# Kernel optimization log

Hardware: AMD Instinct MI355X
Metric: run time of the kernel (lower is better)

## Reference

```python
import jax, jax.numpy as jnp
import numpy as np

NF1, NF2, HEADS = 64, 64, 8
SCALE = (0.5 * (NF1 + NF2)) ** (-0.5)
EPS = 1e-5


def _ln(x, g, b):
    # LayerNorm over last axis
    mu = jnp.mean(x, axis=-1, keepdims=True)
    var = jnp.mean(jnp.square(x - mu), axis=-1, keepdims=True)
    return (x - mu) * jax.lax.rsqrt(var + EPS) * g + b


def setup_inputs() -> dict:
    key = jax.random.key(0)
    ks = jax.random.split(key, 16)
    B, H, W = 4, 256, 256
    s = 0.05
    return {
        "x1": jax.random.normal(ks[0], (B, NF1, H, W), jnp.float32),
        "x2": jax.random.normal(ks[1], (B, NF2, H, W), jnp.float32),
        "q_w": jax.random.normal(ks[2], (HEADS, NF1), jnp.float32) * s,
        "q_b": jnp.zeros((HEADS,), jnp.float32),
        "k_w": jax.random.normal(ks[3], (HEADS, NF2), jnp.float32) * s,
        "k_b": jnp.zeros((HEADS,), jnp.float32),
        "v_w": jax.random.normal(ks[4], (HEADS, NF1), jnp.float32) * s,
        "v_b": jnp.zeros((HEADS,), jnp.float32),
        "bias": jax.random.normal(ks[5], (1, 1, 1, NF2), jnp.float32),
        "sel_w": jax.random.normal(ks[6], (HEADS, NF2), jnp.float32) * s,
        "sel_b": jnp.zeros((HEADS,), jnp.float32),
        "fan_w": jax.random.normal(ks[7], (NF1, HEADS), jnp.float32) * s,
        "fan_b": jnp.zeros((NF1,), jnp.float32),
        "gamma": jax.random.normal(ks[8], (1, NF1, 1, 1), jnp.float32),
        "ln1_w": jnp.ones((NF1,), jnp.float32),
        "ln1_b": jnp.zeros((NF1,), jnp.float32),
        "ln2_w": jnp.ones((NF2,), jnp.float32),
        "ln2_b": jnp.zeros((NF2,), jnp.float32),
    }


def reference(x1, x2, q_w, q_b, k_w, k_b, v_w, v_b, bias, sel_w, sel_b,
              fan_w, fan_b, gamma, ln1_w, ln1_b, ln2_w, ln2_b):
    # Work in NHWC internally (matches the permute(0,2,3,1) pattern).
    x1n = _ln(jnp.transpose(x1, (0, 2, 3, 1)), ln1_w, ln1_b)  # [B,H,W,nf1]
    x2n = _ln(jnp.transpose(x2, (0, 2, 3, 1)), ln2_w, ln2_b)  # [B,H,W,nf2]

    # 1x1 convs == per-pixel linear projections
    q = jnp.einsum('bhwc,dc->bhwd', x1n, q_w) + q_b  # [B,H,W,heads]
    k = jnp.einsum('bhwc,dc->bhwd', x2n, k_w) + k_b  # [B,H,W,heads]
    v = jnp.einsum('bhwc,dc->bhwd', x1n, v_w) + v_b  # [B,H,W,heads]

    # row-wise attention over W: scores [B,H,W,W]
    attn = jax.nn.softmax(SCALE * jnp.einsum('bhwd,bhud->bhwu', q, k), axis=-1)
    mp = jnp.einsum('bhwu,bhud->bhwd', attn, v)  # [B,H,W,heads]

    # bias selector: Linear(nf2 -> heads) applied to learned bias [1,1,1,nf2]
    mp = mp + (jnp.einsum('ijkc,dc->ijkd', bias, sel_w) + sel_b)

    fo = jnp.einsum('bhwd,od->bhwo', mp, fan_w) + fan_b  # [B,H,W,nf1]
    g = jnp.transpose(gamma, (0, 2, 3, 1))  # [1,1,1,nf1]
    out = x1n + g * fo
    return jnp.transpose(out, (0, 3, 1, 2))  # NCHW [B,nf1,H,W]
```

## Files before the change

kernel.cpp:

```cpp
#include <hip/hip_runtime.h>

#define BDIM 512
#define HH 256
#define WW 256
#define NF 64
#define NH 8
#define HW (HH * WW)
#define WBP 68

typedef __attribute__((ext_vector_type(8))) short short8v;
typedef __attribute__((ext_vector_type(4))) float f32x4;

__device__ __forceinline__ unsigned short f2bf(float f) {
  const unsigned u = __float_as_uint(f);
  return (unsigned short)((u + 0x7fffu + ((u >> 16) & 1u)) >> 16);
}

__device__ __forceinline__ uint2 exp2_pack(f32x4 sv) {
  const float e0 = __builtin_amdgcn_exp2f(sv.x);
  const float e1 = __builtin_amdgcn_exp2f(sv.y);
  const float e2 = __builtin_amdgcn_exp2f(sv.z);
  const float e3 = __builtin_amdgcn_exp2f(sv.w);
  uint2 r;
  r.x = (unsigned)f2bf(e0) | ((unsigned)f2bf(e1) << 16);
  r.y = (unsigned)f2bf(e2) | ((unsigned)f2bf(e3) << 16);
  return r;
}

struct __align__(16) Smem {
  unsigned short kb16[WW * 8];
  unsigned short qb16[WW * 8];
  unsigned short vb16[8][264];
  union {
    struct { unsigned short wb1[16 * WBP]; unsigned short wb2[16 * WBP]; } w;
    float mpst[WW][10];
  } u1;
  union {
    unsigned short pstage[8][640];
    float murst2[WW][2];
  } u2;
  float murst[WW][2];
  float Sq1[NH], Sq0[NH], Sk1[NH], Sk0[NH], Sv1[NH], Sv0[NH], bsel[NH];
};

__global__ __launch_bounds__(BDIM, 6)
void cc_attn_kernel(const float* __restrict__ x1,
                    const float* __restrict__ x2,
                    const float* __restrict__ q_w,
                    const float* __restrict__ q_b,
                    const float* __restrict__ k_w,
                    const float* __restrict__ k_b,
                    const float* __restrict__ v_w,
                    const float* __restrict__ v_b,
                    const float* __restrict__ bias,
                    const float* __restrict__ sel_w,
                    const float* __restrict__ sel_b,
                    const float* __restrict__ fan_w,
                    const float* __restrict__ fan_b,
                    const float* __restrict__ gma,
                    const float* __restrict__ ln1w,
                    const float* __restrict__ ln1b,
                    const float* __restrict__ ln2w,
                    const float* __restrict__ ln2b,
                    float* __restrict__ out)
{
  __shared__ Smem s;
  const int tid  = threadIdx.x;
  const int lane = tid & 63;
  const int wid  = tid >> 6;
  const int g    = lane >> 4;
  const int r16  = lane & 15;
  const int b = blockIdx.x >> 8;
  const int h = blockIdx.x & 255;
  const size_t rowbase = ((size_t)(b * NF) * HH + h) * WW;

  const float QS = 0.125f * 1.44269504088896340736f;
  const short8v zero8 = {0,0,0,0,0,0,0,0};
  const f32x4 zero4 = {0.f, 0.f, 0.f, 0.f};

  if (tid < NH) {
    const int d = tid;
    float s1q = 0, s0q = 0, s1k = 0, s0k = 0, s1v = 0, s0v = 0, bs = 0;
    for (int c = 0; c < NF; c++) {
      const float qw = q_w[d * NF + c], kw = k_w[d * NF + c], vw = v_w[d * NF + c];
      s1q += ln1w[c] * qw; s0q += ln1b[c] * qw;
      s1k += ln2w[c] * kw; s0k += ln2b[c] * kw;
      s1v += ln1w[c] * vw; s0v += ln1b[c] * vw;
      bs  += bias[c] * sel_w[d * NF + c];
    }
    s.Sq1[d] = s1q; s.Sq0[d] = s0q + q_b[d];
    s.Sk1[d] = s1k; s.Sk0[d] = s0k + k_b[d];
    s.Sv1[d] = s1v; s.Sv0[d] = s0v + v_b[d];
    s.bsel[d] = bs + sel_b[d];
  }

  for (int i = tid; i < 16 * NF; i += BDIM) {
    const int n = i >> 6, c = i & 63;
    const float w1 = (n < 8 ? q_w[n * NF + c] : v_w[(n - 8) * NF + c]) * ln1w[c];
    const float w2 = (n < 8 ? k_w[n * NF + c] * ln2w[c] : 0.f);
    s.u1.w.wb1[n * WBP + c] = f2bf(w1);
    s.u1.w.wb2[n * WBP + c] = f2bf(w2);
  }

  __syncthreads();

  f32x4 accQV0 = zero4, accQV1 = zero4;
  float s1[2] = {0.f, 0.f}, q1[2] = {0.f, 0.f};

  #pragma unroll 1
  for (int kc = 0; kc < 2; ++kc) {
    const short8v bqv = *reinterpret_cast<const short8v*>(&s.u1.w.wb1[r16 * WBP + kc * 32 + g * 8]);
    #pragma unroll
    for (int m = 0; m < 2; ++m) {
      const int gp = wid * 32 + m * 16 + r16;
      const float* p1 = x1 + rowbase + gp + (size_t)(kc * 32 + g * 8) * HW;
      float xv[8];
      #pragma unroll
      for (int i = 0; i < 8; ++i) xv[i] = p1[(size_t)i * HW];
      unsigned short pk1[8];
      float la = 0.f, lb = 0.f;
      #pragma unroll
      for (int i = 0; i < 8; ++i) { la += xv[i]; lb += xv[i] * xv[i]; pk1[i] = f2bf(xv[i]); }
      s1[m] += la; q1[m] += lb;
      const short8v a1 = *reinterpret_cast<const short8v*>(pk1);
      if (m == 0) accQV0 = __builtin_amdgcn_mfma_f32_16x16x32_bf16(a1, bqv, accQV0, 0, 0, 0);
      else        accQV1 = __builtin_amdgcn_mfma_f32_16x16x32_bf16(a1, bqv, accQV1, 0, 0, 0);
    }
  }

  f32x4 accK0 = zero4, accK1 = zero4;
  float s2[2] = {0.f, 0.f}, q2p[2] = {0.f, 0.f};
  #pragma unroll 1
  for (int kc = 0; kc < 2; ++kc) {
    const short8v bk = *reinterpret_cast<const short8v*>(&s.u1.w.wb2[r16 * WBP + kc * 32 + g * 8]);
    #pragma unroll
    for (int m = 0; m < 2; ++m) {
      const int gp = wid * 32 + m * 16 + r16;
      const float* p2 = x2 + rowbase + gp + (size_t)(kc * 32 + g * 8) * HW;
      float yv[8];
      #pragma unroll
      for (int i = 0; i < 8; ++i) yv[i] = p2[(size_t)i * HW];
      unsigned short pk2[8];
      float lc = 0.f, ld = 0.f;
      #pragma unroll
      for (int i = 0; i < 8; ++i) { lc += yv[i]; ld += yv[i] * yv[i]; pk2[i] = f2bf(yv[i]); }
      s2[m] += lc; q2p[m] += ld;
      const short8v a2 = *reinterpret_cast<const short8v*>(pk2);
      if (m == 0) accK0 = __builtin_amdgcn_mfma_f32_16x16x32_bf16(a2, bk, accK0, 0, 0, 0);
      else        accK1 = __builtin_amdgcn_mfma_f32_16x16x32_bf16(a2, bk, accK1, 0, 0, 0);
    }
  }

  #pragma unroll
  for (int m = 0; m < 2; ++m) {
    float a = s1[m] + __shfl_xor(s1[m], 16);   a += __shfl_xor(a, 32);
    float v = q1[m] + __shfl_xor(q1[m], 16);   v += __shfl_xor(v, 32);
    float c = s2[m] + __shfl_xor(s2[m], 16);   c += __shfl_xor(c, 32);
    float d = q2p[m] + __shfl_xor(q2p[m], 16); d += __shfl_xor(d, 32);
    if (g == 0) {
      const int gp = wid * 32 + m * 16 + r16;
      const float mu1v = a * (1.f / NF);
      s.murst[gp][0] = mu1v;
      s.murst[gp][1] = rsqrtf(v * (1.f / NF) - mu1v * mu1v + 1e-5f);
      const float mu2v = c * (1.f / NF);
      s.u2.murst2[gp][0] = mu2v;
      s.u2.murst2[gp][1] = rsqrtf(d * (1.f / NF) - mu2v * mu2v + 1e-5f);
    }
  }

  __syncthreads();

  #pragma unroll
  for (int m = 0; m < 2; ++m) {
    const f32x4 aQV = m ? accQV1 : accQV0;
    const f32x4 aK  = m ? accK1  : accK0;
    #pragma unroll
    for (int j = 0; j < 4; ++j) {
      const int pix = wid * 32 + m * 16 + g * 4 + j;
      const float mu1v = s.murst[pix][0], rs1v = s.murst[pix][1];
      if (r16 < 8) {
        const float mu2v = s.u2.murst2[pix][0], rs2v = s.u2.murst2[pix][1];
        const float qv = (rs1v * (aQV[j] - mu1v * s.Sq1[r16]) + s.Sq0[r16]) * QS;
        s.qb16[pix * 8 + r16] = f2bf(qv);
        const float kv = rs2v * (aK[j] - mu2v * s.Sk1[r16]) + s.Sk0[r16];
        s.kb16[pix * 8 + r16] = f2bf(kv);
      } else {
        const float vv = rs1v * (aQV[j] - mu1v * s.Sv1[r16 - 8]) + s.Sv0[r16 - 8];
        s.vb16[r16 - 8][pix] = f2bf(vv);
      }
    }
  }

  __syncthreads();

  {
    const int qb0 = wid * 32;
    const short8v ones8 = {(short)0x3F80,(short)0x3F80,(short)0x3F80,(short)0x3F80,
                           (short)0x3F80,(short)0x3F80,(short)0x3F80,(short)0x3F80};

    short8v bq0 = zero8, bq1 = zero8;
    if (g == 0) {
      bq0 = *reinterpret_cast<const short8v*>(&s.qb16[(qb0 + r16) * 8]);
      bq1 = *reinterpret_cast<const short8v*>(&s.qb16[(qb0 + 16 + r16) * 8]);
    }

    f32x4 o0 = zero4, o1 = zero4;
    unsigned short* __restrict__ pst = &s.u2.pstage[wid][0];
    const int wr_off = r16 * 40 + g * 4;
    const int rd_off = r16 * 40 + g * 8;

    #pragma unroll 2
    for (int ch = 0; ch < 8; ++ch) {
      const int u0 = ch * 32;
      short8v ak0 = zero8, ak1 = zero8;
      if (g == 0) {
        ak0 = *reinterpret_cast<const short8v*>(&s.kb16[(u0 + r16) * 8]);
        ak1 = *reinterpret_cast<const short8v*>(&s.kb16[(u0 + 16 + r16) * 8]);
      }
      short8v av = zero8;
      if (r16 < 8)       av = *reinterpret_cast<const short8v*>(&s.vb16[r16][u0 + g * 8]);
      else if (r16 == 8) av = ones8;

      {
        f32x4 s0 = __builtin_amdgcn_mfma_f32_16x16x32_bf16(ak0, bq0, zero4, 0, 0, 0);
        f32x4 s1v = __builtin_amdgcn_mfma_f32_16x16x32_bf16(ak1, bq0, zero4, 0, 0, 0);
        const uint2 p0 = exp2_pack(s0);
        const uint2 p1 = exp2_pack(s1v);
        *reinterpret_cast<uint2*>(&pst[wr_off])      = p0;
        *reinterpret_cast<uint2*>(&pst[wr_off + 16]) = p1;
        const short8v bp = *reinterpret_cast<const short8v*>(&pst[rd_off]);
        o0 = __builtin_amdgcn_mfma_f32_16x16x32_bf16(av, bp, o0, 0, 0, 0);
      }
      {
        f32x4 s0 = __builtin_amdgcn_mfma_f32_16x16x32_bf16(ak0, bq1, zero4, 0, 0, 0);
        f32x4 s1v = __builtin_amdgcn_mfma_f32_16x16x32_bf16(ak1, bq1, zero4, 0, 0, 0);
        const uint2 p0 = exp2_pack(s0);
        const uint2 p1 = exp2_pack(s1v);
        *reinterpret_cast<uint2*>(&pst[wr_off])      = p0;
        *reinterpret_cast<uint2*>(&pst[wr_off + 16]) = p1;
        const short8v bp = *reinterpret_cast<const short8v*>(&pst[rd_off]);
        o1 = __builtin_amdgcn_mfma_f32_16x16x32_bf16(av, bp, o1, 0, 0, 0);
      }
    }

    {
      const int q0 = qb0 + r16;
      const int q1i = qb0 + 16 + r16;
      if (g == 0) {
        *reinterpret_cast<float2*>(&s.u1.mpst[q0][0]) = make_float2(o0.x, o0.y);
        *reinterpret_cast<float2*>(&s.u1.mpst[q0][2]) = make_float2(o0.z, o0.w);
        *reinterpret_cast<float2*>(&s.u1.mpst[q1i][0]) = make_float2(o1.x, o1.y);
        *reinterpret_cast<float2*>(&s.u1.mpst[q1i][2]) = make_float2(o1.z, o1.w);
      } else if (g == 1) {
        *reinterpret_cast<float2*>(&s.u1.mpst[q0][4]) = make_float2(o0.x, o0.y);
        *reinterpret_cast<float2*>(&s.u1.mpst[q0][6]) = make_float2(o0.z, o0.w);
        *reinterpret_cast<float2*>(&s.u1.mpst[q1i][4]) = make_float2(o1.x, o1.y);
        *reinterpret_cast<float2*>(&s.u1.mpst[q1i][6]) = make_float2(o1.z, o1.w);
      } else if (g == 2) {
        s.u1.mpst[q0][8] = o0.x;
        s.u1.mpst[q1i][8] = o1.x;
      }
    }
  }

  __syncthreads();

  {
    const int qg = tid & 255;
    const int role = tid >> 8;
    const float rl = 1.0f / s.u1.mpst[qg][8];
    float mp[NH];
    #pragma unroll
    for (int d = 0; d < NH; d++) mp[d] = s.u1.mpst[qg][d] * rl + s.bsel[d];

    const float m1 = s.murst[qg][0];
    const float r1 = s.murst[qg][1];
    const int c0 = role * 32;
    const size_t qbase = rowbase + qg;
    const float* p = x1 + qbase;
    #pragma unroll 4
    for (int cc = 0; cc < 32; cc++) {
      const int c = c0 + cc;
      float fo = fan_b[c];
      #pragma unroll
      for (int d = 0; d < NH; d++) fo += mp[d] * fan_w[c * NH + d];
      const float xv  = p[(size_t)c * HW];
      const float x1n = (xv - m1) * r1 * ln1w[c] + ln1b[c];
      out[qbase + (size_t)c * HW] = x1n + gma[c] * fo;
    }
  }
}

extern "C" void kernel_launch(void* const* d_in, const int* in_sizes, int n_in,
                              void* d_out, int out_size, void* d_ws, size_t ws_size,
                              hipStream_t stream) {
  (void)in_sizes; (void)n_in; (void)d_ws; (void)ws_size; (void)out_size;
  const float* x1    = (const float*)d_in[0];
  const float* x2    = (const float*)d_in[1];
  const float* q_w   = (const float*)d_in[2];
  const float* q_b   = (const float*)d_in[3];
  const float* k_w   = (const float*)d_in[4];
  const float* k_b   = (const float*)d_in[5];
  const float* v_w   = (const float*)d_in[6];
  const float* v_b   = (const float*)d_in[7];
  const float* bias  = (const float*)d_in[8];
  const float* sel_w = (const float*)d_in[9];
  const float* sel_b = (const float*)d_in[10];
  const float* fan_w = (const float*)d_in[11];
  const float* fan_b = (const float*)d_in[12];
  const float* gma   = (const float*)d_in[13];
  const float* ln1w  = (const float*)d_in[14];
  const float* ln1b  = (const float*)d_in[15];
  const float* ln2w  = (const float*)d_in[16];
  const float* ln2b  = (const float*)d_in[17];

  hipLaunchKernelGGL(cc_attn_kernel, dim3(4 * HH), dim3(BDIM), 0, stream,
                     x1, x2, q_w, q_b, k_w, k_b, v_w, v_b, bias, sel_w, sel_b,
                     fan_w, fan_b, gma, ln1w, ln1b, ln2w, ln2b,
                     (float*)d_out);
}
```

Before: 79.21 us.

## Split fused kernel into projection and attention kernels via workspace

```diff
diff --git a/kernel.cpp b/kernel.cpp
--- a/kernel.cpp
+++ b/kernel.cpp
@@ -1,6 +1,5 @@
 #include <hip/hip_runtime.h>
 
-#define BDIM 512
 #define HH 256
 #define WW 256
 #define NF 64
@@ -15,7 +14,6 @@
   const unsigned u = __float_as_uint(f);
   return (unsigned short)((u + 0x7fffu + ((u >> 16) & 1u)) >> 16);
 }
-
 __device__ __forceinline__ uint2 exp2_pack(f32x4 sv) {
   const float e0 = __builtin_amdgcn_exp2f(sv.x);
   const float e1 = __builtin_amdgcn_exp2f(sv.y);
@@ -27,7 +25,229 @@
   return r;
 }
 
-struct __align__(16) Smem {
+__global__ __launch_bounds__(256, 8)
+void proj_kernel(const float* __restrict__ x1, const float* __restrict__ x2,
+                 const float* __restrict__ q_w, const float* __restrict__ q_b,
+                 const float* __restrict__ k_w, const float* __restrict__ k_b,
+                 const float* __restrict__ v_w, const float* __restrict__ v_b,
+                 const float* __restrict__ bias, const float* __restrict__ sel_w,
+                 const float* __restrict__ sel_b,
+                 const float* __restrict__ ln1w, const float* __restrict__ ln1b,
+                 const float* __restrict__ ln2w, const float* __restrict__ ln2b,
+                 unsigned short* __restrict__ wq, unsigned short* __restrict__ wk,
+                 unsigned short* __restrict__ wv, float2* __restrict__ wst,
+                 float* __restrict__ wbsel)
+{
+  __shared__ float Sq1[NH], Sq0[NH], Sk1[NH], Sk0[NH], Sv1[NH], Sv0[NH];
+  const int tid = threadIdx.x;
+  const int r = blockIdx.x;
+  const int b = r >> 8, h = r & 255;
+
+  if (tid < NH) {
+    const int d = tid;
+    float s1q = 0, s0q = 0, s1k = 0, s0k = 0, s1v = 0, s0v = 0, bs = 0;
+    for (int c = 0; c < NF; c++) {
+      const float qw = q_w[d * NF + c], kw = k_w[d * NF + c], vw = v_w[d * NF + c];
+      s1q += ln1w[c] * qw; s0q += ln1b[c] * qw;
+      s1k += ln2w[c] * kw; s0k += ln2b[c] * kw;
+      s1v += ln1w[c] * vw; s0v += ln1b[c] * vw;
+      bs  += bias[c] * sel_w[d * NF + c];
+    }
+    Sq1[d] = s1q; Sq0[d] = s0q + q_b[d];
+    Sk1[d] = s1k; Sk0[d] = s0k + k_b[d];
+    Sv1[d] = s1v; Sv0[d] = s0v + v_b[d];
+    if (r == 0) wbsel[d] = bs + sel_b[d];
+  }
+  __syncthreads();
+
+  const float QS = 0.125f * 1.44269504088896340736f;
+  const size_t base = ((size_t)(b * NF) * HH + h) * WW + tid;
+  const int pixg = r * 256 + tid;
+
+  {
+    float sum = 0.f, ss = 0.f;
+    float tq[NH] = {}, tv[NH] = {};
+    #pragma unroll 4
+    for (int c = 0; c < NF; c++) {
+      const float xv = x1[base + (size_t)c * HW];
+      sum += xv; ss += xv * xv;
+      const float yv = xv * ln1w[c];
+      #pragma unroll
+      for (int d = 0; d < NH; d++) { tq[d] += yv * q_w[d * NF + c]; tv[d] += yv * v_w[d * NF + c]; }
+    }
+    const float mu = sum * (1.f / NF);
+    const float rstd = rsqrtf(ss * (1.f / NF) - mu * mu + 1e-5f);
+    wst[pixg] = make_float2(mu, rstd);
+    unsigned short pk[8];
+    #pragma unroll
+    for (int d = 0; d < NH; d++) {
+      pk[d] = f2bf((rstd * (tq[d] - mu * Sq1[d]) + Sq0[d]) * QS);
+      wv[r * 2048 + d * 256 + tid] = f2bf(rstd * (tv[d] - mu * Sv1[d]) + Sv0[d]);
+    }
+    *reinterpret_cast<short8v*>(&wq[(size_t)pixg * 8]) = *reinterpret_cast<short8v*>(pk);
+  }
+
+  {
+    float sum = 0.f, ss = 0.f;
+    float tk[NH] = {};
+    #pragma unroll 4
+    for (int c = 0; c < NF; c++) {
+      const float xv = x2[base + (size_t)c * HW];
+      sum += xv; ss += xv * xv;
+      const float yv = xv * ln2w[c];
+      #pragma unroll
+      for (int d = 0; d < NH; d++) tk[d] += yv * k_w[d * NF + c];
+    }
+    const float mu = sum * (1.f / NF);
+    const float rstd = rsqrtf(ss * (1.f / NF) - mu * mu + 1e-5f);
+    unsigned short pk[8];
+    #pragma unroll
+    for (int d = 0; d < NH; d++) pk[d] = f2bf(rstd * (tk[d] - mu * Sk1[d]) + Sk0[d]);
+    *reinterpret_cast<short8v*>(&wk[(size_t)pixg * 8]) = *reinterpret_cast<short8v*>(pk);
+  }
+}
+
+struct __align__(16) SmemB {
+  unsigned short kb16[WW * 8];
+  unsigned short vb16[8][264];
+  unsigned short pstage[8][640];
+  float mpst[WW][10];
+};
+
+__global__ __launch_bounds__(512, 8)
+void attn_kernel(const float* __restrict__ x1,
+                 const float* __restrict__ fan_w, const float* __restrict__ fan_b,
+                 const float* __restrict__ gma,
+                 const float* __restrict__ ln1w, const float* __restrict__ ln1b,
+                 const unsigned short* __restrict__ wq, const unsigned short* __restrict__ wk,
+                 const unsigned short* __restrict__ wv, const float2* __restrict__ wst,
+                 const float* __restrict__ wbsel,
+                 float* __restrict__ out)
+{
+  __shared__ SmemB s;
+  const int tid  = threadIdx.x;
+  const int lane = tid & 63;
+  const int wid  = tid >> 6;
+  const int g    = lane >> 4;
+  const int r16  = lane & 15;
+  const int r = blockIdx.x;
+  const int b = r >> 8, h = r & 255;
+  const size_t rowbase = ((size_t)(b * NF) * HH + h) * WW;
+
+  const short8v zero8 = {0,0,0,0,0,0,0,0};
+  const f32x4 zero4 = {0.f, 0.f, 0.f, 0.f};
+
+  if (tid < 256) {
+    *reinterpret_cast<uint4*>(&s.kb16[tid * 8]) =
+        *reinterpret_cast<const uint4*>(&wk[(size_t)r * 2048 + tid * 8]);
+  } else {
+    const int t = tid - 256;
+    const int d = t >> 5, u0 = (t & 31) * 8;
+    *reinterpret_cast<uint4*>(&s.vb16[d][u0]) =
+        *reinterpret_cast<const uint4*>(&wv[(size_t)r * 2048 + t * 8]);
+  }
+  __syncthreads();
+
+  {
+    const int qb0 = wid * 32;
+    const short8v ones8 = {(short)0x3F80,(short)0x3F80,(short)0x3F80,(short)0x3F80,
+                           (short)0x3F80,(short)0x3F80,(short)0x3F80,(short)0x3F80};
+
+    short8v bq0 = zero8, bq1 = zero8;
+    if (g == 0) {
+      bq0 = *reinterpret_cast<const short8v*>(&wq[((size_t)r * 256 + qb0 + r16) * 8]);
+      bq1 = *reinterpret_cast<const short8v*>(&wq[((size_t)r * 256 + qb0 + 16 + r16) * 8]);
+    }
+
+    f32x4 o0 = zero4, o1 = zero4;
+    unsigned short* __restrict__ pst = &s.pstage[wid][0];
+    const int wr_off = r16 * 40 + g * 4;
+    const int rd_off = r16 * 40 + g * 8;
+
+    #pragma unroll 2
+    for (int ch = 0; ch < 8; ++ch) {
+      const int u0 = ch * 32;
+      short8v ak0 = zero8, ak1 = zero8;
+      if (g == 0) {
+        ak0 = *reinterpret_cast<const short8v*>(&s.kb16[(u0 + r16) * 8]);
+        ak1 = *reinterpret_cast<const short8v*>(&s.kb16[(u0 + 16 + r16) * 8]);
+      }
+      short8v av = zero8;
+      if (r16 < 8)       av = *reinterpret_cast<const short8v*>(&s.vb16[r16][u0 + g * 8]);
+      else if (r16 == 8) av = ones8;
+
+      {
+        f32x4 s0 = __builtin_amdgcn_mfma_f32_16x16x32_bf16(ak0, bq0, zero4, 0, 0, 0);
+        f32x4 s1v = __builtin_amdgcn_mfma_f32_16x16x32_bf16(ak1, bq0, zero4, 0, 0, 0);
+        const uint2 p0 = exp2_pack(s0);
+        const uint2 p1 = exp2_pack(s1v);
+        *reinterpret_cast<uint2*>(&pst[wr_off])      = p0;
+        *reinterpret_cast<uint2*>(&pst[wr_off + 16]) = p1;
+        const short8v bp = *reinterpret_cast<const short8v*>(&pst[rd_off]);
+        o0 = __builtin_amdgcn_mfma_f32_16x16x32_bf16(av, bp, o0, 0, 0, 0);
+      }
+      {
+        f32x4 s0 = __builtin_amdgcn_mfma_f32_16x16x32_bf16(ak0, bq1, zero4, 0, 0, 0);
+        f32x4 s1v = __builtin_amdgcn_mfma_f32_16x16x32_bf16(ak1, bq1, zero4, 0, 0, 0);
+        const uint2 p0 = exp2_pack(s0);
+        const uint2 p1 = exp2_pack(s1v);
+        *reinterpret_cast<uint2*>(&pst[wr_off])      = p0;
+        *reinterpret_cast<uint2*>(&pst[wr_off + 16]) = p1;
+        const short8v bp = *reinterpret_cast<const short8v*>(&pst[rd_off]);
+        o1 = __builtin_amdgcn_mfma_f32_16x16x32_bf16(av, bp, o1, 0, 0, 0);
+      }
+    }
+
+    {
+      const int q0 = qb0 + r16;
+      const int q1i = qb0 + 16 + r16;
+      if (g == 0) {
+        *reinterpret_cast<float2*>(&s.mpst[q0][0]) = make_float2(o0.x, o0.y);
+        *reinterpret_cast<float2*>(&s.mpst[q0][2]) = make_float2(o0.z, o0.w);
+        *reinterpret_cast<float2*>(&s.mpst[q1i][0]) = make_float2(o1.x, o1.y);
+        *reinterpret_cast<float2*>(&s.mpst[q1i][2]) = make_float2(o1.z, o1.w);
+      } else if (g == 1) {
+        *reinterpret_cast<float2*>(&s.mpst[q0][4]) = make_float2(o0.x, o0.y);
+        *reinterpret_cast<float2*>(&s.mpst[q0][6]) = make_float2(o0.z, o0.w);
+        *reinterpret_cast<float2*>(&s.mpst[q1i][4]) = make_float2(o1.x, o1.y);
+        *reinterpret_cast<float2*>(&s.mpst[q1i][6]) = make_float2(o1.z, o1.w);
+      } else if (g == 2) {
+        s.mpst[q0][8] = o0.x;
+        s.mpst[q1i][8] = o1.x;
+      }
+    }
+  }
+
+  __syncthreads();
+
+  {
+    const int qg = tid & 255;
+    const int role = tid >> 8;
+    const float rl = 1.0f / s.mpst[qg][8];
+    float mp[NH];
+    #pragma unroll
+    for (int d = 0; d < NH; d++) mp[d] = s.mpst[qg][d] * rl + wbsel[d];
+
+    const float2 st = wst[(size_t)r * 256 + qg];
+    const float m1 = st.x;
+    const float r1 = st.y;
+    const int c0 = role * 32;
+    const size_t qbase = rowbase + qg;
+    const float* p = x1 + qbase;
+    #pragma unroll 4
+    for (int cc = 0; cc < 32; cc++) {
+      const int c = c0 + cc;
+      float fo = fan_b[c];
+      #pragma unroll
+      for (int d = 0; d < NH; d++) fo += mp[d] * fan_w[c * NH + d];
+      const float xv  = p[(size_t)c * HW];
+      const float x1n = (xv - m1) * r1 * ln1w[c] + ln1b[c];
+      out[qbase + (size_t)c * HW] = x1n + gma[c] * fo;
+    }
+  }
+}
+
+struct __align__(16) SmemF {
   unsigned short kb16[WW * 8];
   unsigned short qb16[WW * 8];
   unsigned short vb16[8][264];
@@ -43,28 +263,20 @@
   float Sq1[NH], Sq0[NH], Sk1[NH], Sk0[NH], Sv1[NH], Sv0[NH], bsel[NH];
 };
 
-__global__ __launch_bounds__(BDIM, 6)
-void cc_attn_kernel(const float* __restrict__ x1,
-                    const float* __restrict__ x2,
-                    const float* __restrict__ q_w,
-                    const float* __restrict__ q_b,
-                    const float* __restrict__ k_w,
-                    const float* __restrict__ k_b,
-                    const float* __restrict__ v_w,
-                    const float* __restrict__ v_b,
-                    const float* __restrict__ bias,
-                    const float* __restrict__ sel_w,
-                    const float* __restrict__ sel_b,
-                    const float* __restrict__ fan_w,
-                    const float* __restrict__ fan_b,
-                    const float* __restrict__ gma,
-                    const float* __restrict__ ln1w,
-                    const float* __restrict__ ln1b,
-                    const float* __restrict__ ln2w,
-                    const float* __restrict__ ln2b,
-                    float* __restrict__ out)
+__global__ __launch_bounds__(512, 8)
+void cc_attn_fused(const float* __restrict__ x1, const float* __restrict__ x2,
+                   const float* __restrict__ q_w, const float* __restrict__ q_b,
+                   const float* __restrict__ k_w, const float* __restrict__ k_b,
+                   const float* __restrict__ v_w, const float* __restrict__ v_b,
+                   const float* __restrict__ bias, const float* __restrict__ sel_w,
+                   const float* __restrict__ sel_b,
+                   const float* __restrict__ fan_w, const float* __restrict__ fan_b,
+                   const float* __restrict__ gma,
+                   const float* __restrict__ ln1w, const float* __restrict__ ln1b,
+                   const float* __restrict__ ln2w, const float* __restrict__ ln2b,
+                   float* __restrict__ out)
 {
-  __shared__ Smem s;
+  __shared__ SmemF s;
   const int tid  = threadIdx.x;
   const int lane = tid & 63;
   const int wid  = tid >> 6;
@@ -93,20 +305,17 @@
     s.Sv1[d] = s1v; s.Sv0[d] = s0v + v_b[d];
     s.bsel[d] = bs + sel_b[d];
   }
-
-  for (int i = tid; i < 16 * NF; i += BDIM) {
+  for (int i = tid; i < 16 * NF; i += 512) {
     const int n = i >> 6, c = i & 63;
     const float w1 = (n < 8 ? q_w[n * NF + c] : v_w[(n - 8) * NF + c]) * ln1w[c];
     const float w2 = (n < 8 ? k_w[n * NF + c] * ln2w[c] : 0.f);
     s.u1.w.wb1[n * WBP + c] = f2bf(w1);
     s.u1.w.wb2[n * WBP + c] = f2bf(w2);
   }
-
   __syncthreads();
 
   f32x4 accQV0 = zero4, accQV1 = zero4;
   float s1[2] = {0.f, 0.f}, q1[2] = {0.f, 0.f};
-
   #pragma unroll 1
   for (int kc = 0; kc < 2; ++kc) {
     const short8v bqv = *reinterpret_cast<const short8v*>(&s.u1.w.wb1[r16 * WBP + kc * 32 + g * 8]);
@@ -127,7 +336,6 @@
       else        accQV1 = __builtin_amdgcn_mfma_f32_16x16x32_bf16(a1, bqv, accQV1, 0, 0, 0);
     }
   }
-
   f32x4 accK0 = zero4, accK1 = zero4;
   float s2[2] = {0.f, 0.f}, q2p[2] = {0.f, 0.f};
   #pragma unroll 1
@@ -150,7 +358,6 @@
       else        accK1 = __builtin_amdgcn_mfma_f32_16x16x32_bf16(a2, bk, accK1, 0, 0, 0);
     }
   }
-
   #pragma unroll
   for (int m = 0; m < 2; ++m) {
     float a = s1[m] + __shfl_xor(s1[m], 16);   a += __shfl_xor(a, 32);
@@ -167,9 +374,7 @@
       s.u2.murst2[gp][1] = rsqrtf(d * (1.f / NF) - mu2v * mu2v + 1e-5f);
     }
   }
-
-  __syncthreads();
-
+  __syncthreads();
   #pragma unroll
   for (int m = 0; m < 2; ++m) {
     const f32x4 aQV = m ? accQV1 : accQV0;
@@ -180,35 +385,27 @@
       const float mu1v = s.murst[pix][0], rs1v = s.murst[pix][1];
       if (r16 < 8) {
         const float mu2v = s.u2.murst2[pix][0], rs2v = s.u2.murst2[pix][1];
-        const float qv = (rs1v * (aQV[j] - mu1v * s.Sq1[r16]) + s.Sq0[r16]) * QS;
-        s.qb16[pix * 8 + r16] = f2bf(qv);
-        const float kv = rs2v * (aK[j] - mu2v * s.Sk1[r16]) + s.Sk0[r16];
-        s.kb16[pix * 8 + r16] = f2bf(kv);
+        s.qb16[pix * 8 + r16] = f2bf((rs1v * (aQV[j] - mu1v * s.Sq1[r16]) + s.Sq0[r16]) * QS);
+        s.kb16[pix * 8 + r16] = f2bf(rs2v * (aK[j] - mu2v * s.Sk1[r16]) + s.Sk0[r16]);
       } else {
-        const float vv = rs1v * (aQV[j] - mu1v * s.Sv1[r16 - 8]) + s.Sv0[r16 - 8];
-        s.vb16[r16 - 8][pix] = f2bf(vv);
-      }
-    }
-  }
-
-  __syncthreads();
-
+        s.vb16[r16 - 8][pix] = f2bf(rs1v * (aQV[j] - mu1v * s.Sv1[r16 - 8]) + s.Sv0[r16 - 8]);
+      }
+    }
+  }
+  __syncthreads();
   {
     const int qb0 = wid * 32;
     const short8v ones8 = {(short)0x3F80,(short)0x3F80,(short)0x3F80,(short)0x3F80,
                            (short)0x3F80,(short)0x3F80,(short)0x3F80,(short)0x3F80};
-
     short8v bq0 = zero8, bq1 = zero8;
     if (g == 0) {
       bq0 = *reinterpret_cast<const short8v*>(&s.qb16[(qb0 + r16) * 8]);
       bq1 = *reinterpret_cast<const short8v*>(&s.qb16[(qb0 + 16 + r16) * 8]);
     }
-
     f32x4 o0 = zero4, o1 = zero4;
     unsigned short* __restrict__ pst = &s.u2.pstage[wid][0];
     const int wr_off = r16 * 40 + g * 4;
     const int rd_off = r16 * 40 + g * 8;
-
     #pragma unroll 2
     for (int ch = 0; ch < 8; ++ch) {
       const int u0 = ch * 32;
@@ -220,7 +417,6 @@
       short8v av = zero8;
       if (r16 < 8)       av = *reinterpret_cast<const short8v*>(&s.vb16[r16][u0 + g * 8]);
       else if (r16 == 8) av = ones8;
-
       {
         f32x4 s0 = __builtin_amdgcn_mfma_f32_16x16x32_bf16(ak0, bq0, zero4, 0, 0, 0);
         f32x4 s1v = __builtin_amdgcn_mfma_f32_16x16x32_bf16(ak1, bq0, zero4, 0, 0, 0);
@@ -242,7 +438,6 @@
         o1 = __builtin_amdgcn_mfma_f32_16x16x32_bf16(av, bp, o1, 0, 0, 0);
       }
     }
-
     {
       const int q0 = qb0 + r16;
       const int q1i = qb0 + 16 + r16;
@@ -262,9 +457,7 @@
       }
     }
   }
-
-  __syncthreads();
-
+  __syncthreads();
   {
     const int qg = tid & 255;
     const int role = tid >> 8;
@@ -272,7 +465,6 @@
     float mp[NH];
     #pragma unroll
     for (int d = 0; d < NH; d++) mp[d] = s.u1.mpst[qg][d] * rl + s.bsel[d];
-
     const float m1 = s.murst[qg][0];
     const float r1 = s.murst[qg][1];
     const int c0 = role * 32;
@@ -294,7 +486,7 @@
 extern "C" void kernel_launch(void* const* d_in, const int* in_sizes, int n_in,
                               void* d_out, int out_size, void* d_ws, size_t ws_size,
                               hipStream_t stream) {
-  (void)in_sizes; (void)n_in; (void)d_ws; (void)ws_size; (void)out_size;
+  (void)in_sizes; (void)n_in; (void)out_size;
   const float* x1    = (const float*)d_in[0];
   const float* x2    = (const float*)d_in[1];
   const float* q_w   = (const float*)d_in[2];
@@ -313,9 +505,27 @@
   const float* ln1b  = (const float*)d_in[15];
   const float* ln2w  = (const float*)d_in[16];
   const float* ln2b  = (const float*)d_in[17];
-
-  hipLaunchKernelGGL(cc_attn_kernel, dim3(4 * HH), dim3(BDIM), 0, stream,
-                     x1, x2, q_w, q_b, k_w, k_b, v_w, v_b, bias, sel_w, sel_b,
-                     fan_w, fan_b, gma, ln1w, ln1b, ln2w, ln2b,
-                     (float*)d_out);
+  float* out = (float*)d_out;
+
+  const size_t NQ = (size_t)1024 * 2048;
+  const size_t WS_NEED = NQ * 2 * 3 + (size_t)1024 * 256 * 8 + 64;
+
+  if (ws_size >= WS_NEED) {
+    unsigned short* wq = (unsigned short*)d_ws;
+    unsigned short* wk = wq + NQ;
+    unsigned short* wv = wk + NQ;
+    float2* wst   = (float2*)(wv + NQ);
+    float*  wbsel = (float*)(wst + (size_t)1024 * 256);
+
+    hipLaunchKernelGGL(proj_kernel, dim3(1024), dim3(256), 0, stream,
+                       x1, x2, q_w, q_b, k_w, k_b, v_w, v_b, bias, sel_w, sel_b,
+                       ln1w, ln1b, ln2w, ln2b, wq, wk, wv, wst, wbsel);
+    hipLaunchKernelGGL(attn_kernel, dim3(1024), dim3(512), 0, stream,
+                       x1, fan_w, fan_b, gma, ln1w, ln1b,
+                       wq, wk, wv, wst, wbsel, out);
+  } else {
+    hipLaunchKernelGGL(cc_attn_fused, dim3(1024), dim3(512), 0, stream,
+                       x1, x2, q_w, q_b, k_w, k_b, v_w, v_b, bias, sel_w, sel_b,
+                       fan_w, fan_b, gma, ln1w, ln1b, ln2w, ln2b, out);
+  }
 }
```

Measured after the change: 90.33 us. 14.0% more time.
